# Optimization experiments

Measured on AMD Instinct MI355X. Metric: run time of the kernel, lower is better.

## Reference

```python
import jax, jax.numpy as jnp
import numpy as np

B, S, E = 1, 4096, 2048
H, HK, D = 16, 4, 128  # num_heads, num_kv_heads, head_dim


def setup_inputs() -> dict:
    key = jax.random.key(0)
    ks = jax.random.split(key, 5)
    sc = 0.02
    return {
        "x": jax.random.normal(ks[0], (B, S, E), dtype=jnp.float32),
        "Wq": jax.random.normal(ks[1], (H * D, E), dtype=jnp.float32) * sc,
        "Wk": jax.random.normal(ks[2], (HK * D, E), dtype=jnp.float32) * sc,
        "Wv": jax.random.normal(ks[3], (HK * D, E), dtype=jnp.float32) * sc,
        "Wo": jax.random.normal(ks[4], (E, H * D), dtype=jnp.float32) * sc,
    }


def reference(x, Wq, Wk, Wv, Wo):
    b, s, _ = x.shape
    # projections (bias=False Linear: x @ W.T), split heads, [B, H, S, D]
    q = (x @ Wq.T).reshape(b, s, H, D).transpose(0, 2, 1, 3).astype(jnp.float16)
    k = (x @ Wk.T).reshape(b, s, HK, D).transpose(0, 2, 1, 3).astype(jnp.float16)
    v = (x @ Wv.T).reshape(b, s, HK, D).transpose(0, 2, 1, 3).astype(jnp.float16)
    # GQA: repeat_interleave kv heads to match query heads
    rep = H // HK
    k = jnp.repeat(k, rep, axis=1)
    v = jnp.repeat(v, rep, axis=1)
    # SDPA in fp32 (non-causal), result cast to half as in torch code
    qf, kf, vf = q.astype(jnp.float32), k.astype(jnp.float32), v.astype(jnp.float32)
    scores = jnp.einsum("bhsd,bhtd->bhst", qf, kf) / np.float32(np.sqrt(D))
    attn = jax.nn.softmax(scores, axis=-1)
    out = jnp.einsum("bhst,bhtd->bhsd", attn, vf).astype(jnp.float16)
    # merge heads and output projection in fp32
    out = out.transpose(0, 2, 1, 3).reshape(b, s, H * D).astype(jnp.float32)
    return out @ Wo.T
```

## Files before the change

### kernel.cpp

```cpp
#include <hip/hip_runtime.h>
#include <stdint.h>

#define SEQ 4096
#define EMB 2048
#define NH 16
#define HDIM 128

typedef _Float16 f16;
typedef _Float16 f16x2 __attribute__((ext_vector_type(2)));
typedef _Float16 f16x4 __attribute__((ext_vector_type(4)));
typedef _Float16 f16x8 __attribute__((ext_vector_type(8)));
typedef float f32x4 __attribute__((ext_vector_type(4)));
typedef unsigned u32x2 __attribute__((ext_vector_type(2)));

#define MFMA16(a, b, c) __builtin_amdgcn_mfma_f32_16x16x32_f16((a), (b), (c), 0, 0, 0)

#define OFF_XH   0ull
#define OFF_WCAT 8388608ull
#define OFF_WHI  14680064ull
#define OFF_WLO  18874368ull
#define OFF_Q    23068672ull
#define OFF_K    31457280ull
#define OFF_VT   33554432ull

__device__ __forceinline__ void gload16(const void* g, void* l) {
    __builtin_amdgcn_global_load_lds((const __attribute__((address_space(1))) unsigned int*)g,
                                     (__attribute__((address_space(3))) unsigned int*)l, 16, 0, 0);
}

__device__ __forceinline__ void swap32p(uint32_t& x, uint32_t& y) {
#if __has_builtin(__builtin_amdgcn_permlane32_swap)
    u32x2 r = __builtin_amdgcn_permlane32_swap(x, y, false, false);
    x = r[0]; y = r[1];
#else
    int l = __lane_id();
    uint32_t xs = (uint32_t)__shfl_xor((int)x, 32, 64), ys = (uint32_t)__shfl_xor((int)y, 32, 64);
    uint32_t nx = (l < 32) ? x : ys;
    uint32_t ny = (l < 32) ? xs : y;
    x = nx; y = ny;
#endif
}
__device__ __forceinline__ void swap16p(uint32_t& x, uint32_t& y) {
#if __has_builtin(__builtin_amdgcn_permlane16_swap)
    u32x2 r = __builtin_amdgcn_permlane16_swap(x, y, false, false);
    x = r[0]; y = r[1];
#else
    int l = __lane_id();
    uint32_t xs = (uint32_t)__shfl_xor((int)x, 16, 64), ys = (uint32_t)__shfl_xor((int)y, 16, 64);
    uint32_t nx = (l & 16) ? ys : x;
    uint32_t ny = (l & 16) ? y : xs;
    x = nx; y = ny;
#endif
}
__device__ __forceinline__ float red_max_lhi(float t) {
    uint32_t a = __float_as_uint(t), b = a;
    swap16p(a, b);
    t = fmaxf(__uint_as_float(a), __uint_as_float(b));
    a = __float_as_uint(t); b = a;
    swap32p(a, b);
    return fmaxf(__uint_as_float(a), __uint_as_float(b));
}
__device__ __forceinline__ float red_sum_lhi(float t) {
    uint32_t a = __float_as_uint(t), b = a;
    swap16p(a, b);
    t = __uint_as_float(a) + __uint_as_float(b);
    a = __float_as_uint(t); b = a;
    swap32p(a, b);
    return __uint_as_float(a) + __uint_as_float(b);
}

__global__ __launch_bounds__(256) void cvt_kernel(
    const float* __restrict__ x, const float* __restrict__ wq,
    const float* __restrict__ wk, const float* __restrict__ wv,
    const float* __restrict__ wo, f16* __restrict__ ws)
{
    int g = blockIdx.x * 256 + threadIdx.x;
    const float* src;
    size_t dst;
    int iswo = 0;
    if (g < 2097152)      { src = x  + (size_t)g * 4;                 dst = OFF_XH + (size_t)g * 4; }
    else if (g < 3145728) { int r = g - 2097152; src = wq + (size_t)r * 4; dst = OFF_WCAT + (size_t)r * 4; }
    else if (g < 3407872) { int r = g - 3145728; src = wk + (size_t)r * 4; dst = OFF_WCAT + 4194304ull + (size_t)r * 4; }
    else if (g < 3670016) { int r = g - 3407872; src = wv + (size_t)r * 4; dst = OFF_WCAT + 5242880ull + (size_t)r * 4; }
    else                  { int r = g - 3670016; src = wo + (size_t)r * 4; dst = OFF_WHI + (size_t)r * 4; iswo = 1; }
    float4 v = *(const float4*)src;
    f16x4 hi;
    hi[0] = (f16)v.x; hi[1] = (f16)v.y; hi[2] = (f16)v.z; hi[3] = (f16)v.w;
    *(f16x4*)&ws[dst] = hi;
    if (iswo) {
        f16x4 lo;
        lo[0] = (f16)(v.x - (float)hi[0]); lo[1] = (f16)(v.y - (float)hi[1]);
        lo[2] = (f16)(v.z - (float)hi[2]); lo[3] = (f16)(v.w - (float)hi[3]);
        *(f16x4*)&ws[dst + (OFF_WLO - OFF_WHI)] = lo;
    }
}

__global__ __launch_bounds__(256) void qkv_gemm(
    const f16* __restrict__ Xh, const f16* __restrict__ Wcat,
    f16* __restrict__ Qb, f16* __restrict__ Kb, f16* __restrict__ Vt)
{
    __shared__ f16 As[128 * 32];
    __shared__ f16 Bs[128 * 32];
    const int tid = threadIdx.x;
    const int lane = tid & 63;
    const int w = tid >> 6;
    const int llo = lane & 15, lhi = lane >> 4;
    const int m0 = blockIdx.y * 128;
    const int n0 = blockIdx.x * 128;
    const int wr = (w >> 1) * 64, wc = (w & 1) * 64;

    f32x4 acc[4][4] = {};

    for (int k0 = 0; k0 < EMB; k0 += 32) {
#pragma unroll
        for (int i = 0; i < 2; ++i) {
            int c = tid + 256 * i;
            gload16(Xh + (size_t)(m0 + (c >> 2)) * EMB + k0 + (c & 3) * 8, &As[c * 8]);
        }
#pragma unroll
        for (int i = 0; i < 2; ++i) {
            int c = tid + 256 * i;
            gload16(Wcat + (size_t)(n0 + (c >> 2)) * EMB + k0 + (c & 3) * 8, &Bs[c * 8]);
        }
        __syncthreads();
        f16x8 af[4], bf[4];
#pragma unroll
        for (int mi = 0; mi < 4; ++mi) af[mi] = *(const f16x8*)&As[(wr + mi * 16 + llo) * 32 + lhi * 8];
#pragma unroll
        for (int ni = 0; ni < 4; ++ni) bf[ni] = *(const f16x8*)&Bs[(wc + ni * 16 + llo) * 32 + lhi * 8];
#pragma unroll
        for (int mi = 0; mi < 4; ++mi)
#pragma unroll
            for (int ni = 0; ni < 4; ++ni)
                acc[mi][ni] = MFMA16(af[mi], bf[ni], acc[mi][ni]);
        __syncthreads();
    }

    if (n0 < 2048) {
#pragma unroll
        for (int mi = 0; mi < 4; ++mi) {
            int m = m0 + wr + mi * 16 + lhi * 4;
#pragma unroll
            for (int ni = 0; ni < 4; ++ni) {
                int n = n0 + wc + ni * 16 + llo;
#pragma unroll
                for (int r = 0; r < 4; ++r)
                    Qb[(size_t)(m + r) * EMB + n] = (f16)acc[mi][ni][r];
            }
        }
    } else if (n0 < 2560) {
#pragma unroll
        for (int mi = 0; mi < 4; ++mi) {
            int m = m0 + wr + mi * 16 + lhi * 4;
#pragma unroll
            for (int ni = 0; ni < 4; ++ni) {
                int n = n0 + wc + ni * 16 + llo - 2048;
#pragma unroll
                for (int r = 0; r < 4; ++r)
                    Kb[(size_t)(m + r) * 512 + n] = (f16)acc[mi][ni][r];
            }
        }
    } else {
#pragma unroll
        for (int mi = 0; mi < 4; ++mi) {
            int mb = m0 + wr + mi * 16 + lhi * 4;
#pragma unroll
            for (int ni = 0; ni < 4; ++ni) {
                int n = n0 + wc + ni * 16 + llo - 2560;
                f16x4 pv;
#pragma unroll
                for (int r = 0; r < 4; ++r) pv[r] = (f16)acc[mi][ni][r];
                *(f16x4*)&Vt[(size_t)n * SEQ + mb] = pv;
            }
        }
    }
}

__global__ __launch_bounds__(256, 2) void attn_kernel(
    const f16* __restrict__ Qb, const f16* __restrict__ Kb, const f16* __restrict__ Vt,
    f16* __restrict__ AO)
{
    __shared__ f16 Ks[2][64 * 128];
    __shared__ f16 Vs[2][128 * 64];
    const int tid = threadIdx.x, lane = tid & 63, w = tid >> 6;
    const int llo = lane & 15, lhi = lane >> 4;
    const int h = blockIdx.y, hk = h >> 2;
    const int wm0 = blockIdx.x * 128 + w * 32;
    const int hcol = h * HDIM;
    const float CS = 0.08838834764831845f * 1.4426950408889634f;

    f16x8 qf[2][4];
#pragma unroll
    for (int G = 0; G < 2; ++G)
#pragma unroll
        for (int kk = 0; kk < 4; ++kk)
            qf[G][kk] = *(const f16x8*)&Qb[(size_t)(wm0 + G * 16 + llo) * EMB + hcol + kk * 32 + lhi * 8];

    const f16* kgp[4];
    const f16* vgp[4];
#pragma unroll
    for (int i = 0; i < 4; ++i) {
        int c = tid + 256 * i;
        int row = c >> 4, cc = (c & 15) ^ (row & 7);
        kgp[i] = Kb + (size_t)row * 512 + hk * HDIM + cc * 8;
    }
#pragma unroll
    for (int i = 0; i < 4; ++i) {
        int c = tid + 256 * i;
        int row = c >> 3, cc = (c & 7) ^ (row & 7);
        vgp[i] = Vt + (size_t)(hk * HDIM + row) * SEQ + cc * 8;
    }

    float mrun[2] = { -3.0e38f, -3.0e38f };
    float lrun[2] = { 0.f, 0.f };
    f32x4 acc[2][8] = {};

    auto stage = [&](int buf, int t0) {
#pragma unroll
        for (int i = 0; i < 4; ++i)
            gload16(kgp[i] + (size_t)t0 * 512, &Ks[buf][(tid + 256 * i) * 8]);
#pragma unroll
        for (int i = 0; i < 4; ++i)
            gload16(vgp[i] + t0, &Vs[buf][(tid + 256 * i) * 8]);
    };

    stage(0, 0);
    __syncthreads();

    for (int tt = 0; tt < 64; ++tt) {
        int cur = tt & 1;
        if (tt < 63) stage(cur ^ 1, (tt + 1) * 64);

        f32x4 s[2][4] = {};
        __builtin_amdgcn_s_setprio(1);
#pragma unroll
        for (int kk = 0; kk < 4; ++kk) {
            f16x8 kf[4];
#pragma unroll
            for (int hh = 0; hh < 4; ++hh) {
                int row = llo + 16 * hh;
                int ccs = (kk * 4 + lhi) ^ (row & 7);
                kf[hh] = *(const f16x8*)&Ks[cur][row * 128 + ccs * 8];
            }
#pragma unroll
            for (int hh = 0; hh < 4; ++hh) {
                s[0][hh] = MFMA16(kf[hh], qf[0][kk], s[0][hh]);
                s[1][hh] = MFMA16(kf[hh], qf[1][kk], s[1][hh]);
            }
        }
        __builtin_amdgcn_s_setprio(0);

        float tm[2];
#pragma unroll
        for (int G = 0; G < 2; ++G) {
            float t = -3.0e38f;
#pragma unroll
            for (int hh = 0; hh < 4; ++hh)
#pragma unroll
                for (int r = 0; r < 4; ++r) { float v = s[G][hh][r] * CS; s[G][hh][r] = v; t = fmaxf(t, v); }
            tm[G] = red_max_lhi(t);
        }
        int need = (tm[0] > mrun[0]) || (tm[1] > mrun[1]);
        if (__any(need)) {
#pragma unroll
            for (int G = 0; G < 2; ++G) {
                float mnew = fmaxf(mrun[G], tm[G]);
                float alpha = __builtin_amdgcn_exp2f(mrun[G] - mnew);
                mrun[G] = mnew; lrun[G] *= alpha;
                float ar[4];
#pragma unroll
                for (int r = 0; r < 4; ++r) ar[r] = __shfl(alpha, lhi * 4 + r, 64);
#pragma unroll
                for (int ni = 0; ni < 8; ++ni)
#pragma unroll
                    for (int r = 0; r < 4; ++r) acc[G][ni][r] *= ar[r];
            }
        }

        union F2U { f16x2 h; uint32_t u; };
        uint32_t Y[2][4][2];
#pragma unroll
        for (int G = 0; G < 2; ++G) {
            float ts = 0.f;
#pragma unroll
            for (int hh = 0; hh < 4; ++hh) {
#pragma unroll
                for (int r = 0; r < 4; ++r) { float p = __builtin_amdgcn_exp2f(s[G][hh][r] - mrun[G]); s[G][hh][r] = p; ts += p; }
                F2U a, b;
                a.h[0] = (f16)s[G][hh][0]; a.h[1] = (f16)s[G][hh][1];
                b.h[0] = (f16)s[G][hh][2]; b.h[1] = (f16)s[G][hh][3];
                Y[G][hh][0] = a.u; Y[G][hh][1] = b.u;
            }
            lrun[G] += red_sum_lhi(ts);
        }

        f16x8 paf[2][2];
#pragma unroll
        for (int G = 0; G < 2; ++G)
#pragma unroll
            for (int c = 0; c < 2; ++c) {
                union { f16x8 v; uint32_t u[4]; } pa;
#pragma unroll
                for (int jj = 0; jj < 2; ++jj) {
                    uint32_t xa = Y[G][2 * c][jj], xb = Y[G][2 * c + 1][jj];
                    swap32p(xa, xb);
                    swap16p(xa, xb);
                    pa.u[jj] = xa; pa.u[2 + jj] = xb;
                }
                paf[G][c] = pa.v;
            }

        __builtin_amdgcn_s_setprio(1);
#pragma unroll
        for (int c = 0; c < 2; ++c)
#pragma unroll
            for (int ni = 0; ni < 8; ++ni) {
                int d = ni * 16 + llo;
                f16x8 vf = *(const f16x8*)&Vs[cur][d * 64 + (((4 * c + lhi) ^ (d & 7)) * 8)];
                acc[0][ni] = MFMA16(paf[0][c], vf, acc[0][ni]);
                acc[1][ni] = MFMA16(paf[1][c], vf, acc[1][ni]);
            }
        __builtin_amdgcn_s_setprio(0);

        __syncthreads();
    }

#pragma unroll
    for (int G = 0; G < 2; ++G) {
        float linv = 1.0f / lrun[G];
        float lr[4];
#pragma unroll
        for (int r = 0; r < 4; ++r) lr[r] = __shfl(linv, lhi * 4 + r, 64);
#pragma unroll
        for (int ni = 0; ni < 8; ++ni) {
            int n = hcol + ni * 16 + llo;
#pragma unroll
            for (int r = 0; r < 4; ++r)
                AO[(size_t)(wm0 + G * 16 + lhi * 4 + r) * EMB + n] = (f16)(acc[G][ni][r] * lr[r]);
        }
    }
}

__global__ __launch_bounds__(256) void o_gemm(
    const f16* __restrict__ A, const f16* __restrict__ Whi, const f16* __restrict__ Wlo,
    float* __restrict__ Co)
{
    __shared__ f16 As[128 * 32];
    __shared__ f16 Bh[128 * 32];
    __shared__ f16 Bl[128 * 32];
    const int tid = threadIdx.x;
    const int lane = tid & 63;
    const int w = tid >> 6;
    const int llo = lane & 15, lhi = lane >> 4;
    const int m0 = blockIdx.y * 128;
    const int n0 = blockIdx.x * 128;
    const int wr = (w >> 1) * 64, wc = (w & 1) * 64;

    f32x4 acc[4][4] = {};

    for (int k0 = 0; k0 < EMB; k0 += 32) {
#pragma unroll
        for (int i = 0; i < 2; ++i) {
            int c = tid + 256 * i;
            gload16(A + (size_t)(m0 + (c >> 2)) * EMB + k0 + (c & 3) * 8, &As[c * 8]);
        }
#pragma unroll
        for (int i = 0; i < 2; ++i) {
            int c = tid + 256 * i;
            gload16(Whi + (size_t)(n0 + (c >> 2)) * EMB + k0 + (c & 3) * 8, &Bh[c * 8]);
        }
#pragma unroll
        for (int i = 0; i < 2; ++i) {
            int c = tid + 256 * i;
            gload16(Wlo + (size_t)(n0 + (c >> 2)) * EMB + k0 + (c & 3) * 8, &Bl[c * 8]);
        }
        __syncthreads();
        f16x8 af[4], bh[4], bl[4];
#pragma unroll
        for (int mi = 0; mi < 4; ++mi) af[mi] = *(const f16x8*)&As[(wr + mi * 16 + llo) * 32 + lhi * 8];
#pragma unroll
        for (int ni = 0; ni < 4; ++ni) bh[ni] = *(const f16x8*)&Bh[(wc + ni * 16 + llo) * 32 + lhi * 8];
#pragma unroll
        for (int ni = 0; ni < 4; ++ni) bl[ni] = *(const f16x8*)&Bl[(wc + ni * 16 + llo) * 32 + lhi * 8];
#pragma unroll
        for (int mi = 0; mi < 4; ++mi)
#pragma unroll
            for (int ni = 0; ni < 4; ++ni) {
                acc[mi][ni] = MFMA16(af[mi], bh[ni], acc[mi][ni]);
                acc[mi][ni] = MFMA16(af[mi], bl[ni], acc[mi][ni]);
            }
        __syncthreads();
    }

#pragma unroll
    for (int mi = 0; mi < 4; ++mi) {
        int m = m0 + wr + mi * 16 + lhi * 4;
#pragma unroll
        for (int ni = 0; ni < 4; ++ni) {
            int n = n0 + wc + ni * 16 + llo;
#pragma unroll
            for (int r = 0; r < 4; ++r)
                Co[(size_t)(m + r) * EMB + n] = acc[mi][ni][r];
        }
    }
}

extern "C" void kernel_launch(void* const* d_in, const int* in_sizes, int n_in,
                              void* d_out, int out_size, void* d_ws, size_t ws_size,
                              hipStream_t stream) {
    const float* x  = (const float*)d_in[0];
    const float* wq = (const float*)d_in[1];
    const float* wk = (const float*)d_in[2];
    const float* wv = (const float*)d_in[3];
    const float* wo = (const float*)d_in[4];
    f16* ws = (f16*)d_ws;

    f16* Xh   = ws + OFF_XH;
    f16* Wcat = ws + OFF_WCAT;
    f16* Whi  = ws + OFF_WHI;
    f16* Wlo  = ws + OFF_WLO;
    f16* Qb   = ws + OFF_Q;
    f16* Kb   = ws + OFF_K;
    f16* Vt   = ws + OFF_VT;

    cvt_kernel<<<18432, 256, 0, stream>>>(x, wq, wk, wv, wo, ws);
    qkv_gemm<<<dim3(24, 32), 256, 0, stream>>>(Xh, Wcat, Qb, Kb, Vt);
    attn_kernel<<<dim3(32, 16), 256, 0, stream>>>(Qb, Kb, Vt, Xh );
    o_gemm<<<dim3(16, 32), 256, 0, stream>>>(Xh , Whi, Wlo, (float*)d_out);
}
```

Measured before the change: 430.9 us.

## Drop Wo hi/lo split, fold softmax scale into Q, restructure attention to 8 waves

The output projection now uses a single fp16 copy of Wo instead of a hi+lo split, which halves that GEMM's MFMA work and B-tile loads at some cost in accuracy. The softmax scale is folded into Q when the QKV GEMM stores it, removing a per-score multiply in attention. The attention kernel moves to 512 threads, each wave handling 16 query rows instead of 32. It also skips the running-max rescale unless the max grows by more than 8 in log2 units, and defers the row-sum reduction across lanes to the end. These steps cut per-tile work and register pressure, but they lose the Q-fragment reuse across two row groups and add a small numerical risk.

```diff
diff --git a/kernel.cpp b/kernel.cpp
--- a/kernel.cpp
+++ b/kernel.cpp
@@ -17,8 +17,7 @@
 
 #define OFF_XH   0ull
 #define OFF_WCAT 8388608ull
-#define OFF_WHI  14680064ull
-#define OFF_WLO  18874368ull
+#define OFF_WO   14680064ull
 #define OFF_Q    23068672ull
 #define OFF_K    31457280ull
 #define OFF_VT   33554432ull
@@ -77,22 +76,15 @@
     int g = blockIdx.x * 256 + threadIdx.x;
     const float* src;
     size_t dst;
-    int iswo = 0;
     if (g < 2097152)      { src = x  + (size_t)g * 4;                 dst = OFF_XH + (size_t)g * 4; }
     else if (g < 3145728) { int r = g - 2097152; src = wq + (size_t)r * 4; dst = OFF_WCAT + (size_t)r * 4; }
     else if (g < 3407872) { int r = g - 3145728; src = wk + (size_t)r * 4; dst = OFF_WCAT + 4194304ull + (size_t)r * 4; }
     else if (g < 3670016) { int r = g - 3407872; src = wv + (size_t)r * 4; dst = OFF_WCAT + 5242880ull + (size_t)r * 4; }
-    else                  { int r = g - 3670016; src = wo + (size_t)r * 4; dst = OFF_WHI + (size_t)r * 4; iswo = 1; }
+    else                  { int r = g - 3670016; src = wo + (size_t)r * 4; dst = OFF_WO + (size_t)r * 4; }
     float4 v = *(const float4*)src;
-    f16x4 hi;
-    hi[0] = (f16)v.x; hi[1] = (f16)v.y; hi[2] = (f16)v.z; hi[3] = (f16)v.w;
-    *(f16x4*)&ws[dst] = hi;
-    if (iswo) {
-        f16x4 lo;
-        lo[0] = (f16)(v.x - (float)hi[0]); lo[1] = (f16)(v.y - (float)hi[1]);
-        lo[2] = (f16)(v.z - (float)hi[2]); lo[3] = (f16)(v.w - (float)hi[3]);
-        *(f16x4*)&ws[dst + (OFF_WLO - OFF_WHI)] = lo;
-    }
+    f16x4 hv;
+    hv[0] = (f16)v.x; hv[1] = (f16)v.y; hv[2] = (f16)v.z; hv[3] = (f16)v.w;
+    *(f16x4*)&ws[dst] = hv;
 }
 
 __global__ __launch_bounds__(256) void qkv_gemm(
@@ -108,6 +100,7 @@
     const int m0 = blockIdx.y * 128;
     const int n0 = blockIdx.x * 128;
     const int wr = (w >> 1) * 64, wc = (w & 1) * 64;
+    const float CS = 0.08838834764831845f * 1.4426950408889634f;
 
     f32x4 acc[4][4] = {};
 
@@ -145,7 +138,7 @@
                 int n = n0 + wc + ni * 16 + llo;
 #pragma unroll
                 for (int r = 0; r < 4; ++r)
-                    Qb[(size_t)(m + r) * EMB + n] = (f16)acc[mi][ni][r];
+                    Qb[(size_t)(m + r) * EMB + n] = (f16)(acc[mi][ni][r] * CS);
             }
         }
     } else if (n0 < 2560) {
@@ -176,7 +169,7 @@
     }
 }
 
-__global__ __launch_bounds__(256, 2) void attn_kernel(
+__global__ __launch_bounds__(512, 4) void attn_kernel(
     const f16* __restrict__ Qb, const f16* __restrict__ Kb, const f16* __restrict__ Vt,
     f16* __restrict__ AO)
 {
@@ -185,43 +178,40 @@
     const int tid = threadIdx.x, lane = tid & 63, w = tid >> 6;
     const int llo = lane & 15, lhi = lane >> 4;
     const int h = blockIdx.y, hk = h >> 2;
-    const int wm0 = blockIdx.x * 128 + w * 32;
+    const int wm0 = blockIdx.x * 128 + w * 16;
     const int hcol = h * HDIM;
-    const float CS = 0.08838834764831845f * 1.4426950408889634f;
-
-    f16x8 qf[2][4];
-#pragma unroll
-    for (int G = 0; G < 2; ++G)
-#pragma unroll
-        for (int kk = 0; kk < 4; ++kk)
-            qf[G][kk] = *(const f16x8*)&Qb[(size_t)(wm0 + G * 16 + llo) * EMB + hcol + kk * 32 + lhi * 8];
-
-    const f16* kgp[4];
-    const f16* vgp[4];
-#pragma unroll
-    for (int i = 0; i < 4; ++i) {
-        int c = tid + 256 * i;
+
+    f16x8 qf[4];
+#pragma unroll
+    for (int kk = 0; kk < 4; ++kk)
+        qf[kk] = *(const f16x8*)&Qb[(size_t)(wm0 + llo) * EMB + hcol + kk * 32 + lhi * 8];
+
+    const f16* kgp[2];
+    const f16* vgp[2];
+#pragma unroll
+    for (int i = 0; i < 2; ++i) {
+        int c = tid + 512 * i;
         int row = c >> 4, cc = (c & 15) ^ (row & 7);
         kgp[i] = Kb + (size_t)row * 512 + hk * HDIM + cc * 8;
     }
 #pragma unroll
-    for (int i = 0; i < 4; ++i) {
-        int c = tid + 256 * i;
+    for (int i = 0; i < 2; ++i) {
+        int c = tid + 512 * i;
         int row = c >> 3, cc = (c & 7) ^ (row & 7);
         vgp[i] = Vt + (size_t)(hk * HDIM + row) * SEQ + cc * 8;
     }
 
-    float mrun[2] = { -3.0e38f, -3.0e38f };
-    float lrun[2] = { 0.f, 0.f };
-    f32x4 acc[2][8] = {};
+    float mrun = -3.0e38f;
+    float lsum = 0.f;
+    f32x4 acc[8] = {};
 
     auto stage = [&](int buf, int t0) {
 #pragma unroll
-        for (int i = 0; i < 4; ++i)
-            gload16(kgp[i] + (size_t)t0 * 512, &Ks[buf][(tid + 256 * i) * 8]);
-#pragma unroll
-        for (int i = 0; i < 4; ++i)
-            gload16(vgp[i] + t0, &Vs[buf][(tid + 256 * i) * 8]);
+        for (int i = 0; i < 2; ++i)
+            gload16(kgp[i] + (size_t)t0 * 512, &Ks[buf][(tid + 512 * i) * 8]);
+#pragma unroll
+        for (int i = 0; i < 2; ++i)
+            gload16(vgp[i] + t0, &Vs[buf][(tid + 512 * i) * 8]);
     };
 
     stage(0, 0);
@@ -231,7 +221,7 @@
         int cur = tt & 1;
         if (tt < 63) stage(cur ^ 1, (tt + 1) * 64);
 
-        f32x4 s[2][4] = {};
+        f32x4 s[4] = {};
         __builtin_amdgcn_s_setprio(1);
 #pragma unroll
         for (int kk = 0; kk < 4; ++kk) {
@@ -243,72 +233,58 @@
                 kf[hh] = *(const f16x8*)&Ks[cur][row * 128 + ccs * 8];
             }
 #pragma unroll
-            for (int hh = 0; hh < 4; ++hh) {
-                s[0][hh] = MFMA16(kf[hh], qf[0][kk], s[0][hh]);
-                s[1][hh] = MFMA16(kf[hh], qf[1][kk], s[1][hh]);
-            }
+            for (int hh = 0; hh < 4; ++hh)
+                s[hh] = MFMA16(kf[hh], qf[kk], s[hh]);
         }
         __builtin_amdgcn_s_setprio(0);
 
-        float tm[2];
-#pragma unroll
-        for (int G = 0; G < 2; ++G) {
-            float t = -3.0e38f;
-#pragma unroll
-            for (int hh = 0; hh < 4; ++hh)
-#pragma unroll
-                for (int r = 0; r < 4; ++r) { float v = s[G][hh][r] * CS; s[G][hh][r] = v; t = fmaxf(t, v); }
-            tm[G] = red_max_lhi(t);
-        }
-        int need = (tm[0] > mrun[0]) || (tm[1] > mrun[1]);
-        if (__any(need)) {
-#pragma unroll
-            for (int G = 0; G < 2; ++G) {
-                float mnew = fmaxf(mrun[G], tm[G]);
-                float alpha = __builtin_amdgcn_exp2f(mrun[G] - mnew);
-                mrun[G] = mnew; lrun[G] *= alpha;
-                float ar[4];
-#pragma unroll
-                for (int r = 0; r < 4; ++r) ar[r] = __shfl(alpha, lhi * 4 + r, 64);
-#pragma unroll
-                for (int ni = 0; ni < 8; ++ni)
-#pragma unroll
-                    for (int r = 0; r < 4; ++r) acc[G][ni][r] *= ar[r];
-            }
+        float t = -3.0e38f;
+#pragma unroll
+        for (int hh = 0; hh < 4; ++hh)
+#pragma unroll
+            for (int r = 0; r < 4; ++r) t = fmaxf(t, s[hh][r]);
+        float tm = red_max_lhi(t);
+
+        if (__any(tm > mrun + 8.f)) {
+            float mnew = fmaxf(mrun, tm);
+            float alpha = __builtin_amdgcn_exp2f(mrun - mnew);
+            mrun = mnew; lsum *= alpha;
+            float ar[4];
+#pragma unroll
+            for (int r = 0; r < 4; ++r) ar[r] = __shfl(alpha, lhi * 4 + r, 64);
+#pragma unroll
+            for (int ni = 0; ni < 8; ++ni)
+#pragma unroll
+                for (int r = 0; r < 4; ++r) acc[ni][r] *= ar[r];
         }
 
         union F2U { f16x2 h; uint32_t u; };
-        uint32_t Y[2][4][2];
-#pragma unroll
-        for (int G = 0; G < 2; ++G) {
-            float ts = 0.f;
-#pragma unroll
-            for (int hh = 0; hh < 4; ++hh) {
-#pragma unroll
-                for (int r = 0; r < 4; ++r) { float p = __builtin_amdgcn_exp2f(s[G][hh][r] - mrun[G]); s[G][hh][r] = p; ts += p; }
-                F2U a, b;
-                a.h[0] = (f16)s[G][hh][0]; a.h[1] = (f16)s[G][hh][1];
-                b.h[0] = (f16)s[G][hh][2]; b.h[1] = (f16)s[G][hh][3];
-                Y[G][hh][0] = a.u; Y[G][hh][1] = b.u;
-            }
-            lrun[G] += red_sum_lhi(ts);
-        }
-
-        f16x8 paf[2][2];
-#pragma unroll
-        for (int G = 0; G < 2; ++G)
-#pragma unroll
-            for (int c = 0; c < 2; ++c) {
-                union { f16x8 v; uint32_t u[4]; } pa;
-#pragma unroll
-                for (int jj = 0; jj < 2; ++jj) {
-                    uint32_t xa = Y[G][2 * c][jj], xb = Y[G][2 * c + 1][jj];
-                    swap32p(xa, xb);
-                    swap16p(xa, xb);
-                    pa.u[jj] = xa; pa.u[2 + jj] = xb;
-                }
-                paf[G][c] = pa.v;
-            }
+        uint32_t Y[4][2];
+        float ts = 0.f;
+#pragma unroll
+        for (int hh = 0; hh < 4; ++hh) {
+#pragma unroll
+            for (int r = 0; r < 4; ++r) { float p = __builtin_amdgcn_exp2f(s[hh][r] - mrun); s[hh][r] = p; ts += p; }
+            F2U a, b;
+            a.h[0] = (f16)s[hh][0]; a.h[1] = (f16)s[hh][1];
+            b.h[0] = (f16)s[hh][2]; b.h[1] = (f16)s[hh][3];
+            Y[hh][0] = a.u; Y[hh][1] = b.u;
+        }
+        lsum += ts;
+
+        f16x8 paf[2];
+#pragma unroll
+        for (int c = 0; c < 2; ++c) {
+            union { f16x8 v; uint32_t u[4]; } pa;
+#pragma unroll
+            for (int jj = 0; jj < 2; ++jj) {
+                uint32_t xa = Y[2 * c][jj], xb = Y[2 * c + 1][jj];
+                swap32p(xa, xb);
+                swap16p(xa, xb);
+                pa.u[jj] = xa; pa.u[2 + jj] = xb;
+            }
+            paf[c] = pa.v;
+        }
 
         __builtin_amdgcn_s_setprio(1);
 #pragma unroll
@@ -317,37 +293,32 @@
             for (int ni = 0; ni < 8; ++ni) {
                 int d = ni * 16 + llo;
                 f16x8 vf = *(const f16x8*)&Vs[cur][d * 64 + (((4 * c + lhi) ^ (d & 7)) * 8)];
-                acc[0][ni] = MFMA16(paf[0][c], vf, acc[0][ni]);
-                acc[1][ni] = MFMA16(paf[1][c], vf, acc[1][ni]);
+                acc[ni] = MFMA16(paf[c], vf, acc[ni]);
             }
         __builtin_amdgcn_s_setprio(0);
 
         __syncthreads();
     }
 
-#pragma unroll
-    for (int G = 0; G < 2; ++G) {
-        float linv = 1.0f / lrun[G];
-        float lr[4];
-#pragma unroll
-        for (int r = 0; r < 4; ++r) lr[r] = __shfl(linv, lhi * 4 + r, 64);
-#pragma unroll
-        for (int ni = 0; ni < 8; ++ni) {
-            int n = hcol + ni * 16 + llo;
-#pragma unroll
-            for (int r = 0; r < 4; ++r)
-                AO[(size_t)(wm0 + G * 16 + lhi * 4 + r) * EMB + n] = (f16)(acc[G][ni][r] * lr[r]);
-        }
+    float linv = 1.0f / red_sum_lhi(lsum);
+    float lr[4];
+#pragma unroll
+    for (int r = 0; r < 4; ++r) lr[r] = __shfl(linv, lhi * 4 + r, 64);
+#pragma unroll
+    for (int ni = 0; ni < 8; ++ni) {
+        int n = hcol + ni * 16 + llo;
+#pragma unroll
+        for (int r = 0; r < 4; ++r)
+            AO[(size_t)(wm0 + lhi * 4 + r) * EMB + n] = (f16)(acc[ni][r] * lr[r]);
     }
 }
 
 __global__ __launch_bounds__(256) void o_gemm(
-    const f16* __restrict__ A, const f16* __restrict__ Whi, const f16* __restrict__ Wlo,
+    const f16* __restrict__ A, const f16* __restrict__ Bw,
     float* __restrict__ Co)
 {
     __shared__ f16 As[128 * 32];
-    __shared__ f16 Bh[128 * 32];
-    __shared__ f16 Bl[128 * 32];
+    __shared__ f16 Bs[128 * 32];
     const int tid = threadIdx.x;
     const int lane = tid & 63;
     const int w = tid >> 6;
@@ -367,28 +338,19 @@
 #pragma unroll
         for (int i = 0; i < 2; ++i) {
             int c = tid + 256 * i;
-            gload16(Whi + (size_t)(n0 + (c >> 2)) * EMB + k0 + (c & 3) * 8, &Bh[c * 8]);
-        }
-#pragma unroll
-        for (int i = 0; i < 2; ++i) {
-            int c = tid + 256 * i;
-            gload16(Wlo + (size_t)(n0 + (c >> 2)) * EMB + k0 + (c & 3) * 8, &Bl[c * 8]);
-        }
-        __syncthreads();
-        f16x8 af[4], bh[4], bl[4];
+            gload16(Bw + (size_t)(n0 + (c >> 2)) * EMB + k0 + (c & 3) * 8, &Bs[c * 8]);
+        }
+        __syncthreads();
+        f16x8 af[4], bf[4];
 #pragma unroll
         for (int mi = 0; mi < 4; ++mi) af[mi] = *(const f16x8*)&As[(wr + mi * 16 + llo) * 32 + lhi * 8];
 #pragma unroll
-        for (int ni = 0; ni < 4; ++ni) bh[ni] = *(const f16x8*)&Bh[(wc + ni * 16 + llo) * 32 + lhi * 8];
-#pragma unroll
-        for (int ni = 0; ni < 4; ++ni) bl[ni] = *(const f16x8*)&Bl[(wc + ni * 16 + llo) * 32 + lhi * 8];
+        for (int ni = 0; ni < 4; ++ni) bf[ni] = *(const f16x8*)&Bs[(wc + ni * 16 + llo) * 32 + lhi * 8];
 #pragma unroll
         for (int mi = 0; mi < 4; ++mi)
 #pragma unroll
-            for (int ni = 0; ni < 4; ++ni) {
-                acc[mi][ni] = MFMA16(af[mi], bh[ni], acc[mi][ni]);
-                acc[mi][ni] = MFMA16(af[mi], bl[ni], acc[mi][ni]);
-            }
+            for (int ni = 0; ni < 4; ++ni)
+                acc[mi][ni] = MFMA16(af[mi], bf[ni], acc[mi][ni]);
         __syncthreads();
     }
 
@@ -417,14 +379,13 @@
 
     f16* Xh   = ws + OFF_XH;
     f16* Wcat = ws + OFF_WCAT;
-    f16* Whi  = ws + OFF_WHI;
-    f16* Wlo  = ws + OFF_WLO;
+    f16* Wo16 = ws + OFF_WO;
     f16* Qb   = ws + OFF_Q;
     f16* Kb   = ws + OFF_K;
     f16* Vt   = ws + OFF_VT;
 
     cvt_kernel<<<18432, 256, 0, stream>>>(x, wq, wk, wv, wo, ws);
     qkv_gemm<<<dim3(24, 32), 256, 0, stream>>>(Xh, Wcat, Qb, Kb, Vt);
-    attn_kernel<<<dim3(32, 16), 256, 0, stream>>>(Qb, Kb, Vt, Xh );
-    o_gemm<<<dim3(16, 32), 256, 0, stream>>>(Xh , Whi, Wlo, (float*)d_out);
-}
+    attn_kernel<<<dim3(32, 16), 512, 0, stream>>>(Qb, Kb, Vt, Xh );
+    o_gemm<<<dim3(16, 32), 256, 0, stream>>>(Xh , Wo16, (float*)d_out);
+}
```

After: 385.6 us. -10.5%, faster.
